# Optimization experiments

Measured on AMD Instinct MI355X. Metric: run time of the kernel, lower is better.

Reference implementation:

```python
import jax, jax.numpy as jnp
import numpy as np

N, E, D, K = 100000, 1000000, 64, 2  # nodes, edges, channels, kernel_size (dim=1, degree=1)


def setup_inputs() -> dict:
    key = jax.random.key(0)
    ks = jax.random.split(key, 10)
    x = jax.random.normal(ks[0], (N, D), dtype=jnp.float32)
    edge_index = jax.random.randint(ks[1], (2, E), 0, N, dtype=jnp.int64)
    edge_attr = jax.random.uniform(ks[2], (E, 1), dtype=jnp.float32)
    s = 1.0 / np.sqrt(D)
    W1 = jax.random.uniform(ks[3], (K, D, D), jnp.float32, -s, s)   # spline weights layer1 [K, in, out]
    lw1 = jax.random.uniform(ks[4], (D, D), jnp.float32, -s, s)     # root linear (x @ lw)
    b1 = jnp.zeros((D,), jnp.float32)
    W2 = jax.random.uniform(ks[5], (K, D, D), jnp.float32, -s, s)
    lw2 = jax.random.uniform(ks[6], (D, D), jnp.float32, -s, s)
    b2 = jnp.zeros((D,), jnp.float32)
    return {"x": x, "edge_index": edge_index, "edge_attr": edge_attr,
            "W1": W1, "lw1": lw1, "b1": b1, "W2": W2, "lw2": lw2, "b2": b2}


def spline_conv(x, src, dst, u, W, lw, b):
    # dim=1, degree=1, open B-spline: v = u*(K-1); linear interp between kernels floor(v), floor(v)+1
    k = W.shape[0]
    v = u[:, 0] * (k - 1)
    i0 = jnp.clip(jnp.floor(v), 0, k - 1).astype(jnp.int32)
    frac = v - i0.astype(v.dtype)            # in [0,1); 0 at u==1 after clipping
    i1 = jnp.minimum(i0 + 1, k - 1)
    Z = jnp.einsum('ni,kio->nko', x, W)      # [N, K, out] precompute per-kernel transforms
    msg = (1.0 - frac)[:, None] * Z[src, i0] + frac[:, None] * Z[src, i1]  # [E, out]
    agg = jax.ops.segment_sum(msg, dst, num_segments=x.shape[0])
    cnt = jax.ops.segment_sum(jnp.ones_like(dst, dtype=x.dtype), dst, num_segments=x.shape[0])
    out = agg / jnp.maximum(cnt, 1.0)[:, None]   # mean aggregation
    return out + x @ lw + b                      # root weight + bias


def reference(x, edge_index, edge_attr, W1, lw1, b1, W2, lw2, b2):
    src, dst = edge_index[0], edge_index[1]
    h = spline_conv(x, src, dst, edge_attr, W1, lw1, b1)
    h = jax.nn.relu(h)                 # dropout is identity in eval mode
    h = spline_conv(h, src, dst, edge_attr, W2, lw2, b2)
    h = jax.nn.relu(h)
    return h
```

## Files before the change

### kernel.cpp

```cpp
#include <hip/hip_runtime.h>

#define TPB 256

typedef __attribute__((ext_vector_type(8))) short bf16x8;
typedef __attribute__((ext_vector_type(4))) float f32x4;

__device__ __forceinline__ float bf2f(unsigned short u) {
    unsigned int x = ((unsigned int)u) << 16;
    return __builtin_bit_cast(float, x);
}
__device__ __forceinline__ unsigned short f2bf(float f) {
    unsigned int u = __builtin_bit_cast(unsigned int, f);
    unsigned int r = u + 0x7FFFu + ((u >> 16) & 1u);
    return (unsigned short)(r >> 16);
}

__global__ void prep_kernel(const float* __restrict__ x, uint2* __restrict__ xb, int n4,
                            const float* __restrict__ W1, const float* __restrict__ lw1,
                            const float* __restrict__ W2, const float* __restrict__ lw2,
                            bf16x8* __restrict__ WA,
                            const int* __restrict__ dst, const int* __restrict__ src,
                            const float* __restrict__ u, int* __restrict__ counts,
                            uint2* __restrict__ cp, int E) {
    int t = blockIdx.x * TPB + threadIdx.x;
    if (t < 3072) {
        int which = t / 1536;
        int rem = t - which * 1536;
        int fragid = rem >> 6;
        int lane = rem & 63;
        int kk = fragid >> 2, ct = fragid & 3;
        const float* W  = which ? W2  : W1;
        const float* lw = which ? lw2 : lw1;
        int col = ct * 16 + (lane & 15);
        int kbase = kk * 32 + (lane >> 4) * 8;
        short vals[8];
#pragma unroll
        for (int j = 0; j < 8; ++j) {
            int k = kbase + j;
            float v = (k < 128) ? W[(k & 1) * 4096 + (k >> 1) * 64 + col]
                                : lw[(k - 128) * 64 + col];
            vals[j] = (short)f2bf(v);
        }
        WA[t] = *reinterpret_cast<bf16x8*>(vals);
    }
    if (t < n4) {
        float4 v = reinterpret_cast<const float4*>(x)[t];
        uint2 r;
        r.x = (unsigned int)f2bf(v.x) | ((unsigned int)f2bf(v.y) << 16);
        r.y = (unsigned int)f2bf(v.z) | ((unsigned int)f2bf(v.w) << 16);
        xb[t] = r;
    }
    if (t < E) {
        int d = dst[t];
        int r = atomicAdd(&counts[d], 1);
        unsigned int uq = (unsigned int)__float2int_rn(u[t] * 32767.f);
        cp[t] = make_uint2((unsigned int)d | ((unsigned int)r << 17),
                           (unsigned int)src[t] | (uq << 17));
    }
}

__global__ void scan1_kernel(const int* __restrict__ counts, int* __restrict__ offsets,
                             int* __restrict__ bsum, int n) {
    __shared__ int s[TPB];
    int t = threadIdx.x;
    int base = blockIdx.x * 1024 + t * 4;
    int v[4];
#pragma unroll
    for (int q = 0; q < 4; ++q) v[q] = (base + q < n) ? counts[base + q] : 0;
    int tsum = v[0] + v[1] + v[2] + v[3];
    s[t] = tsum;
    __syncthreads();
    for (int off = 1; off < TPB; off <<= 1) {
        int x = (t >= off) ? s[t - off] : 0;
        __syncthreads();
        s[t] += x;
        __syncthreads();
    }
    int acc = s[t] - tsum;
#pragma unroll
    for (int q = 0; q < 4; ++q) {
        if (base + q < n) offsets[base + q] = acc;
        acc += v[q];
    }
    if (t == TPB - 1) bsum[blockIdx.x] = s[TPB - 1];
}

__global__ void scan2_kernel(int* __restrict__ bsum, int nblk) {
    __shared__ int s[TPB];
    int t = threadIdx.x;
    int v = (t < nblk) ? bsum[t] : 0;
    s[t] = v;
    __syncthreads();
    for (int off = 1; off < TPB; off <<= 1) {
        int x = (t >= off) ? s[t - off] : 0;
        __syncthreads();
        s[t] += x;
        __syncthreads();
    }
    if (t < nblk) bsum[t] = s[t] - v;
}

__global__ void scan3_kernel(int* __restrict__ offsets, const int* __restrict__ bsum,
                             int n, int E) {
    int base = blockIdx.x * 1024 + threadIdx.x * 4;
    int add = bsum[blockIdx.x];
#pragma unroll
    for (int q = 0; q < 4; ++q) {
        int idx = base + q;
        if (idx < n) offsets[idx] += add;
    }
    if (blockIdx.x == 0 && threadIdx.x == 0) offsets[n] = E;
}

__global__ void fill_kernel(const uint2* __restrict__ cp,
                            const int* __restrict__ offsets,
                            unsigned int* __restrict__ csr, int E, int nphases) {
    int stride = gridDim.x * TPB;
    for (int p = 0; p < nphases; ++p) {
        for (int e = blockIdx.x * TPB + threadIdx.x; e < E; e += stride) {
            uint2 r = cp[e];
            int d = r.x & 0x1FFFF;
            if ((d >> 16) == p) {
                int pos = offsets[d] + (int)(r.x >> 17);
                csr[pos] = r.y;
            }
        }
    }
}

__global__ void agg_kernel(const unsigned int* __restrict__ featu,
                           const int* __restrict__ offsets,
                           const unsigned int* __restrict__ csr,
                           unsigned int* __restrict__ A, int N) {
    int gw = (blockIdx.x * TPB + threadIdx.x) >> 6;
    int lane = threadIdx.x & 63;
    int n0 = gw * 2;
    if (n0 >= N) return;
    int half = lane >> 5, sub = lane & 31;
    const float us = 1.f / 32767.f;

    int ov = offsets[min(n0 + (lane & 3), N)];
    int o0 = __shfl(ov, 0), o1 = __shfl(ov, 1), o2 = __shfl(ov, 2);
    int beg = o0;
    int cnt = o2 - o0;
    unsigned int cw = (lane < cnt) ? csr[beg + lane] : 0u;

    int S0 = 0, E0 = o1 - o0;
    int S1 = E0, E1 = cnt;

    unsigned int fb[16], cs[16];
#pragma unroll
    for (int i = 0; i < 2; ++i) {
        int si = i ? S1 : S0;
        int ei = i ? E1 : E0;
        int bend = min(min(ei, si + 16), 64);
#pragma unroll
        for (int q = 0; q < 8; ++q) {
            int eidx = si + 2 * q + half;
            bool v = eidx < bend;
            unsigned int c = __shfl(cw, v ? eidx : 0);
            cs[i * 8 + q] = c;
            fb[i * 8 + q] = featu[(size_t)(c & 0x1FFFF) * 32 + sub];
        }
    }

#pragma unroll
    for (int i = 0; i < 2; ++i) {
        int si = i ? S1 : S0;
        int ei = i ? E1 : E0;
        int bend = min(min(ei, si + 16), 64);
        float a0x = 0.f, a1x = 0.f, a0y = 0.f, a1y = 0.f;
#pragma unroll
        for (int q = 0; q < 8; ++q) {
            int eidx = si + 2 * q + half;
            float m = (eidx < bend) ? 1.f : 0.f;
            unsigned int c = cs[i * 8 + q];
            unsigned int f = fb[i * 8 + q];
            float uu = (float)(c >> 17) * us;
            float w1 = uu * m;
            float w0 = m - w1;
            float fx = bf2f((unsigned short)f);
            float fy = bf2f((unsigned short)(f >> 16));
            a0x = fmaf(fx, w0, a0x); a1x = fmaf(fx, w1, a1x);
            a0y = fmaf(fy, w0, a0y); a1y = fmaf(fy, w1, a1y);
        }
        int tstart = max(si, bend);
        for (int t = tstart + half; t < ei; t += 2) {
            unsigned int c = csr[beg + t];
            unsigned int f = featu[(size_t)(c & 0x1FFFF) * 32 + sub];
            float uu = (float)(c >> 17) * us;
            float w0 = 1.f - uu;
            float fx = bf2f((unsigned short)f);
            float fy = bf2f((unsigned short)(f >> 16));
            a0x = fmaf(fx, w0, a0x); a1x = fmaf(fx, uu, a1x);
            a0y = fmaf(fy, w0, a0y); a1y = fmaf(fy, uu, a1y);
        }
        a0x += __shfl_xor(a0x, 32); a1x += __shfl_xor(a1x, 32);
        a0y += __shfl_xor(a0y, 32); a1y += __shfl_xor(a1y, 32);
        int node = n0 + i;
        int cN = ei - si;
        float inv = 1.f / (float)(cN > 0 ? cN : 1);
        if (half == 0 && node < N) {
            uint2 pk;
            pk.x = (unsigned int)f2bf(a0x * inv) | ((unsigned int)f2bf(a1x * inv) << 16);
            pk.y = (unsigned int)f2bf(a0y * inv) | ((unsigned int)f2bf(a1y * inv) << 16);
            *reinterpret_cast<uint2*>(A + (size_t)node * 64 + sub * 2) = pk;
        }
    }
}

__global__ void gemm_mfma_kernel(const unsigned int* __restrict__ A,
                                 const unsigned short* __restrict__ feat,
                                 const bf16x8* __restrict__ WA,
                                 const float* __restrict__ bias,
                                 unsigned short* __restrict__ out_bf,
                                 float* __restrict__ out_f,
                                 int N, int write_f32) {
    int w = threadIdx.x >> 6, lane = threadIdx.x & 63;
    int node = blockIdx.x * 64 + w * 16 + (lane & 15);
    int nc = min(node, N - 1);
    int kq = lane >> 4;
    const char* arow = (const char*)A + (size_t)nc * 256 + kq * 16;
    const char* frow = (const char*)feat + (size_t)nc * 128 + kq * 16;
    bf16x8 bq[6];
    bq[0] = *(const bf16x8*)(arow);
    bq[1] = *(const bf16x8*)(arow + 64);
    bq[2] = *(const bf16x8*)(arow + 128);
    bq[3] = *(const bf16x8*)(arow + 192);
    bq[4] = *(const bf16x8*)(frow);
    bq[5] = *(const bf16x8*)(frow + 64);

    f32x4 acc0 = {0.f, 0.f, 0.f, 0.f}, acc1 = acc0, acc2 = acc0, acc3 = acc0;
#pragma unroll
    for (int kk = 0; kk < 6; ++kk) {
        bf16x8 b = bq[kk];
        acc0 = __builtin_amdgcn_mfma_f32_16x16x32_bf16(WA[(kk * 4 + 0) * 64 + lane], b, acc0, 0, 0, 0);
        acc1 = __builtin_amdgcn_mfma_f32_16x16x32_bf16(WA[(kk * 4 + 1) * 64 + lane], b, acc1, 0, 0, 0);
        acc2 = __builtin_amdgcn_mfma_f32_16x16x32_bf16(WA[(kk * 4 + 2) * 64 + lane], b, acc2, 0, 0, 0);
        acc3 = __builtin_amdgcn_mfma_f32_16x16x32_bf16(WA[(kk * 4 + 3) * 64 + lane], b, acc3, 0, 0, 0);
    }
    if (node >= N) return;

    f32x4 accs[4] = {acc0, acc1, acc2, acc3};
    int cb_hi = 4 * kq;
#pragma unroll
    for (int ct = 0; ct < 4; ++ct) {
        int cb = ct * 16 + cb_hi;
        float r0 = fmaxf(accs[ct][0] + bias[cb + 0], 0.f);
        float r1 = fmaxf(accs[ct][1] + bias[cb + 1], 0.f);
        float r2 = fmaxf(accs[ct][2] + bias[cb + 2], 0.f);
        float r3 = fmaxf(accs[ct][3] + bias[cb + 3], 0.f);
        if (write_f32) {
            *reinterpret_cast<float4*>(out_f + (size_t)node * 64 + cb) =
                make_float4(r0, r1, r2, r3);
        } else {
            uint2 pk;
            pk.x = (unsigned int)f2bf(r0) | ((unsigned int)f2bf(r1) << 16);
            pk.y = (unsigned int)f2bf(r2) | ((unsigned int)f2bf(r3) << 16);
            *reinterpret_cast<uint2*>(out_bf + (size_t)node * 64 + cb) = pk;
        }
    }
}

extern "C" void kernel_launch(void* const* d_in, const int* in_sizes, int n_in,
                              void* d_out, int out_size, void* d_ws, size_t ws_size,
                              hipStream_t stream) {
    const float* x   = (const float*)d_in[0];
    const int*   ei  = (const int*)d_in[1];
    const float* ea  = (const float*)d_in[2];
    const float* W1  = (const float*)d_in[3];
    const float* lw1 = (const float*)d_in[4];
    const float* b1  = (const float*)d_in[5];
    const float* W2  = (const float*)d_in[6];
    const float* lw2 = (const float*)d_in[7];
    const float* b2  = (const float*)d_in[8];

    const int N = in_sizes[0] / 64;
    const int E = in_sizes[1] / 2;

    char* p = (char*)d_ws;
    auto carve = [&](size_t bytes) -> void* {
        void* r = (void*)p;
        p += (bytes + 255) & ~(size_t)255;
        return r;
    };
    unsigned short* xb   = (unsigned short*)carve((size_t)N * 64 * 2);
    unsigned short* h    = (unsigned short*)carve((size_t)N * 64 * 2);
    unsigned int*   A    = (unsigned int*)carve((size_t)N * 64 * 4);
    bf16x8* WA      = (bf16x8*)carve(3072 * 16);
    int*   counts   = (int*)carve((size_t)N * 4);
    int*   offsets  = (int*)carve((size_t)(N + 1) * 4);
    int*   bsum     = (int*)carve(256 * 4);
    uint2* cp       = (uint2*)carve((size_t)E * 8);
    unsigned int* csr = (unsigned int*)carve((size_t)E * 4);

    const int* src = ei;
    const int* dst = ei + E;

    hipMemsetAsync(counts, 0, (size_t)N * 4, stream);

    int n4 = N * 64 / 4;
    int prepTotal = n4 > E ? n4 : E;
    prep_kernel<<<(prepTotal + TPB - 1) / TPB, TPB, 0, stream>>>(
        x, (uint2*)xb, n4, W1, lw1, W2, lw2, WA, dst, src, ea, counts, cp, E);

    int nscan = (N + 1023) / 1024;
    scan1_kernel<<<nscan, TPB, 0, stream>>>(counts, offsets, bsum, N);
    scan2_kernel<<<1, TPB, 0, stream>>>(bsum, nscan);
    scan3_kernel<<<nscan, TPB, 0, stream>>>(offsets, bsum, N, E);

    int eBlocks = (E + TPB - 1) / TPB;
    int nphases = (N + 65535) >> 16;
    fill_kernel<<<eBlocks, TPB, 0, stream>>>(cp, offsets, csr, E, nphases);

    int nwaves = (N + 1) / 2;
    int aBlocks = (nwaves + 3) / 4;
    int gBlocks = (N + 63) / 64;

    agg_kernel<<<aBlocks, TPB, 0, stream>>>((const unsigned int*)xb, offsets, csr, A, N);
    gemm_mfma_kernel<<<gBlocks, TPB, 0, stream>>>(A, xb, WA, b1, h, nullptr, N, 0);
    agg_kernel<<<aBlocks, TPB, 0, stream>>>((const unsigned int*)h, offsets, csr, A, N);
    gemm_mfma_kernel<<<gBlocks, TPB, 0, stream>>>(A, h, WA + 1536, b2, nullptr, (float*)d_out, N, 1);
}
```

Before: 166.8 us.

## Fuse neighbor aggregation with MFMA GEMM via LDS staging per 16-node block

Merges the aggregation and MFMA GEMM kernels into one. Each 256-thread block aggregates 16 nodes into shared memory, then each wave computes one 16-column output tile from LDS. This removes the global round trip of the N×64 intermediate A buffer and two kernel launches per layer. In exchange each wave now runs only 16x16 MFMA tiles, adds a block-wide barrier, and the GEMM phase uses less parallel work per block.

```diff
diff --git a/kernel.cpp b/kernel.cpp
--- a/kernel.cpp
+++ b/kernel.cpp
@@ -128,137 +128,125 @@
     }
 }
 
-__global__ void agg_kernel(const unsigned int* __restrict__ featu,
-                           const int* __restrict__ offsets,
-                           const unsigned int* __restrict__ csr,
-                           unsigned int* __restrict__ A, int N) {
-    int gw = (blockIdx.x * TPB + threadIdx.x) >> 6;
-    int lane = threadIdx.x & 63;
-    int n0 = gw * 2;
-    if (n0 >= N) return;
+__global__ void fused_kernel(const unsigned int* __restrict__ featu,
+                             const int* __restrict__ offsets,
+                             const unsigned int* __restrict__ csr,
+                             const bf16x8* __restrict__ WA,
+                             const float* __restrict__ bias,
+                             unsigned short* __restrict__ out_bf,
+                             float* __restrict__ out_f,
+                             int N, int write_f32) {
+    __shared__ unsigned int lds[16 * 68];
+    int wid = threadIdx.x >> 6, lane = threadIdx.x & 63;
+    int nb = blockIdx.x * 16;
     int half = lane >> 5, sub = lane & 31;
     const float us = 1.f / 32767.f;
 
-    int ov = offsets[min(n0 + (lane & 3), N)];
-    int o0 = __shfl(ov, 0), o1 = __shfl(ov, 1), o2 = __shfl(ov, 2);
-    int beg = o0;
-    int cnt = o2 - o0;
-    unsigned int cw = (lane < cnt) ? csr[beg + lane] : 0u;
-
-    int S0 = 0, E0 = o1 - o0;
-    int S1 = E0, E1 = cnt;
-
-    unsigned int fb[16], cs[16];
-#pragma unroll
-    for (int i = 0; i < 2; ++i) {
-        int si = i ? S1 : S0;
-        int ei = i ? E1 : E0;
-        int bend = min(min(ei, si + 16), 64);
-#pragma unroll
-        for (int q = 0; q < 8; ++q) {
-            int eidx = si + 2 * q + half;
-            bool v = eidx < bend;
-            unsigned int c = __shfl(cw, v ? eidx : 0);
-            cs[i * 8 + q] = c;
-            fb[i * 8 + q] = featu[(size_t)(c & 0x1FFFF) * 32 + sub];
+#pragma unroll
+    for (int batch = 0; batch < 2; ++batch) {
+        int n0 = nb + wid * 4 + batch * 2;
+        int ov = offsets[min(n0 + (lane & 3), N)];
+        int o0 = __shfl(ov, 0), o1 = __shfl(ov, 1), o2 = __shfl(ov, 2);
+        int beg = o0;
+        int cnt = o2 - o0;
+        unsigned int cw = (lane < cnt) ? csr[beg + lane] : 0u;
+        int S0 = 0, E0 = o1 - o0, S1 = E0, E1 = cnt;
+
+        unsigned int fb[16], cs[16];
+#pragma unroll
+        for (int i = 0; i < 2; ++i) {
+            int si = i ? S1 : S0;
+            int ei = i ? E1 : E0;
+            int bend = min(min(ei, si + 16), 64);
+#pragma unroll
+            for (int q = 0; q < 8; ++q) {
+                int eidx = si + 2 * q + half;
+                bool v = eidx < bend;
+                unsigned int c = __shfl(cw, v ? eidx : 0);
+                cs[i * 8 + q] = c;
+                fb[i * 8 + q] = featu[(size_t)(c & 0x1FFFF) * 32 + sub];
+            }
         }
-    }
-
-#pragma unroll
-    for (int i = 0; i < 2; ++i) {
-        int si = i ? S1 : S0;
-        int ei = i ? E1 : E0;
-        int bend = min(min(ei, si + 16), 64);
-        float a0x = 0.f, a1x = 0.f, a0y = 0.f, a1y = 0.f;
-#pragma unroll
-        for (int q = 0; q < 8; ++q) {
-            int eidx = si + 2 * q + half;
-            float m = (eidx < bend) ? 1.f : 0.f;
-            unsigned int c = cs[i * 8 + q];
-            unsigned int f = fb[i * 8 + q];
-            float uu = (float)(c >> 17) * us;
-            float w1 = uu * m;
-            float w0 = m - w1;
-            float fx = bf2f((unsigned short)f);
-            float fy = bf2f((unsigned short)(f >> 16));
-            a0x = fmaf(fx, w0, a0x); a1x = fmaf(fx, w1, a1x);
-            a0y = fmaf(fy, w0, a0y); a1y = fmaf(fy, w1, a1y);
+
+#pragma unroll
+        for (int i = 0; i < 2; ++i) {
+            int si = i ? S1 : S0;
+            int ei = i ? E1 : E0;
+            int bend = min(min(ei, si + 16), 64);
+            float a0x = 0.f, a1x = 0.f, a0y = 0.f, a1y = 0.f;
+#pragma unroll
+            for (int q = 0; q < 8; ++q) {
+                int eidx = si + 2 * q + half;
+                float m = (eidx < bend) ? 1.f : 0.f;
+                unsigned int c = cs[i * 8 + q];
+                unsigned int f = fb[i * 8 + q];
+                float uu = (float)(c >> 17) * us;
+                float w1 = uu * m;
+                float w0 = m - w1;
+                float fx = bf2f((unsigned short)f);
+                float fy = bf2f((unsigned short)(f >> 16));
+                a0x = fmaf(fx, w0, a0x); a1x = fmaf(fx, w1, a1x);
+                a0y = fmaf(fy, w0, a0y); a1y = fmaf(fy, w1, a1y);
+            }
+            int tstart = max(si, bend);
+            for (int t = tstart + half; t < ei; t += 2) {
+                unsigned int c = csr[beg + t];
+                unsigned int f = featu[(size_t)(c & 0x1FFFF) * 32 + sub];
+                float uu = (float)(c >> 17) * us;
+                float w0 = 1.f - uu;
+                float fx = bf2f((unsigned short)f);
+                float fy = bf2f((unsigned short)(f >> 16));
+                a0x = fmaf(fx, w0, a0x); a1x = fmaf(fx, uu, a1x);
+                a0y = fmaf(fy, w0, a0y); a1y = fmaf(fy, uu, a1y);
+            }
+            a0x += __shfl_xor(a0x, 32); a1x += __shfl_xor(a1x, 32);
+            a0y += __shfl_xor(a0y, 32); a1y += __shfl_xor(a1y, 32);
+            int cN = ei - si;
+            float inv = 1.f / (float)(cN > 0 ? cN : 1);
+            if (half == 0) {
+                int nrel = n0 + i - nb;
+                uint2 pk;
+                pk.x = (unsigned int)f2bf(a0x * inv) | ((unsigned int)f2bf(a1x * inv) << 16);
+                pk.y = (unsigned int)f2bf(a0y * inv) | ((unsigned int)f2bf(a1y * inv) << 16);
+                *reinterpret_cast<uint2*>(&lds[nrel * 68 + sub * 2]) = pk;
+            }
         }
-        int tstart = max(si, bend);
-        for (int t = tstart + half; t < ei; t += 2) {
-            unsigned int c = csr[beg + t];
-            unsigned int f = featu[(size_t)(c & 0x1FFFF) * 32 + sub];
-            float uu = (float)(c >> 17) * us;
-            float w0 = 1.f - uu;
-            float fx = bf2f((unsigned short)f);
-            float fy = bf2f((unsigned short)(f >> 16));
-            a0x = fmaf(fx, w0, a0x); a1x = fmaf(fx, uu, a1x);
-            a0y = fmaf(fy, w0, a0y); a1y = fmaf(fy, uu, a1y);
-        }
-        a0x += __shfl_xor(a0x, 32); a1x += __shfl_xor(a1x, 32);
-        a0y += __shfl_xor(a0y, 32); a1y += __shfl_xor(a1y, 32);
-        int node = n0 + i;
-        int cN = ei - si;
-        float inv = 1.f / (float)(cN > 0 ? cN : 1);
-        if (half == 0 && node < N) {
-            uint2 pk;
-            pk.x = (unsigned int)f2bf(a0x * inv) | ((unsigned int)f2bf(a1x * inv) << 16);
-            pk.y = (unsigned int)f2bf(a0y * inv) | ((unsigned int)f2bf(a1y * inv) << 16);
-            *reinterpret_cast<uint2*>(A + (size_t)node * 64 + sub * 2) = pk;
-        }
-    }
-}
-
-__global__ void gemm_mfma_kernel(const unsigned int* __restrict__ A,
-                                 const unsigned short* __restrict__ feat,
-                                 const bf16x8* __restrict__ WA,
-                                 const float* __restrict__ bias,
-                                 unsigned short* __restrict__ out_bf,
-                                 float* __restrict__ out_f,
-                                 int N, int write_f32) {
-    int w = threadIdx.x >> 6, lane = threadIdx.x & 63;
-    int node = blockIdx.x * 64 + w * 16 + (lane & 15);
+    }
+    __syncthreads();
+
+    int node = nb + (lane & 15);
     int nc = min(node, N - 1);
     int kq = lane >> 4;
-    const char* arow = (const char*)A + (size_t)nc * 256 + kq * 16;
-    const char* frow = (const char*)feat + (size_t)nc * 128 + kq * 16;
+    const unsigned int* arow = &lds[(lane & 15) * 68 + kq * 4];
+    const char* frow = (const char*)featu + (size_t)nc * 128 + kq * 16;
     bf16x8 bq[6];
-    bq[0] = *(const bf16x8*)(arow);
-    bq[1] = *(const bf16x8*)(arow + 64);
-    bq[2] = *(const bf16x8*)(arow + 128);
-    bq[3] = *(const bf16x8*)(arow + 192);
-    bq[4] = *(const bf16x8*)(frow);
-    bq[5] = *(const bf16x8*)(frow + 64);
-
-    f32x4 acc0 = {0.f, 0.f, 0.f, 0.f}, acc1 = acc0, acc2 = acc0, acc3 = acc0;
-#pragma unroll
-    for (int kk = 0; kk < 6; ++kk) {
-        bf16x8 b = bq[kk];
-        acc0 = __builtin_amdgcn_mfma_f32_16x16x32_bf16(WA[(kk * 4 + 0) * 64 + lane], b, acc0, 0, 0, 0);
-        acc1 = __builtin_amdgcn_mfma_f32_16x16x32_bf16(WA[(kk * 4 + 1) * 64 + lane], b, acc1, 0, 0, 0);
-        acc2 = __builtin_amdgcn_mfma_f32_16x16x32_bf16(WA[(kk * 4 + 2) * 64 + lane], b, acc2, 0, 0, 0);
-        acc3 = __builtin_amdgcn_mfma_f32_16x16x32_bf16(WA[(kk * 4 + 3) * 64 + lane], b, acc3, 0, 0, 0);
-    }
+    bq[0] = *reinterpret_cast<const bf16x8*>(arow);
+    bq[1] = *reinterpret_cast<const bf16x8*>(arow + 16);
+    bq[2] = *reinterpret_cast<const bf16x8*>(arow + 32);
+    bq[3] = *reinterpret_cast<const bf16x8*>(arow + 48);
+    bq[4] = *reinterpret_cast<const bf16x8*>(frow);
+    bq[5] = *reinterpret_cast<const bf16x8*>(frow + 64);
+
+    f32x4 acc = {0.f, 0.f, 0.f, 0.f};
+#pragma unroll
+    for (int kk = 0; kk < 6; ++kk)
+        acc = __builtin_amdgcn_mfma_f32_16x16x32_bf16(WA[(kk * 4 + wid) * 64 + lane],
+                                                      bq[kk], acc, 0, 0, 0);
     if (node >= N) return;
 
-    f32x4 accs[4] = {acc0, acc1, acc2, acc3};
-    int cb_hi = 4 * kq;
-#pragma unroll
-    for (int ct = 0; ct < 4; ++ct) {
-        int cb = ct * 16 + cb_hi;
-        float r0 = fmaxf(accs[ct][0] + bias[cb + 0], 0.f);
-        float r1 = fmaxf(accs[ct][1] + bias[cb + 1], 0.f);
-        float r2 = fmaxf(accs[ct][2] + bias[cb + 2], 0.f);
-        float r3 = fmaxf(accs[ct][3] + bias[cb + 3], 0.f);
-        if (write_f32) {
-            *reinterpret_cast<float4*>(out_f + (size_t)node * 64 + cb) =
-                make_float4(r0, r1, r2, r3);
-        } else {
-            uint2 pk;
-            pk.x = (unsigned int)f2bf(r0) | ((unsigned int)f2bf(r1) << 16);
-            pk.y = (unsigned int)f2bf(r2) | ((unsigned int)f2bf(r3) << 16);
-            *reinterpret_cast<uint2*>(out_bf + (size_t)node * 64 + cb) = pk;
-        }
+    int cb = wid * 16 + 4 * kq;
+    float r0 = fmaxf(acc[0] + bias[cb + 0], 0.f);
+    float r1 = fmaxf(acc[1] + bias[cb + 1], 0.f);
+    float r2 = fmaxf(acc[2] + bias[cb + 2], 0.f);
+    float r3 = fmaxf(acc[3] + bias[cb + 3], 0.f);
+    if (write_f32) {
+        *reinterpret_cast<float4*>(out_f + (size_t)node * 64 + cb) =
+            make_float4(r0, r1, r2, r3);
+    } else {
+        uint2 pk;
+        pk.x = (unsigned int)f2bf(r0) | ((unsigned int)f2bf(r1) << 16);
+        pk.y = (unsigned int)f2bf(r2) | ((unsigned int)f2bf(r3) << 16);
+        *reinterpret_cast<uint2*>(out_bf + (size_t)node * 64 + cb) = pk;
     }
 }
 
@@ -286,7 +274,6 @@
     };
     unsigned short* xb   = (unsigned short*)carve((size_t)N * 64 * 2);
     unsigned short* h    = (unsigned short*)carve((size_t)N * 64 * 2);
-    unsigned int*   A    = (unsigned int*)carve((size_t)N * 64 * 4);
     bf16x8* WA      = (bf16x8*)carve(3072 * 16);
     int*   counts   = (int*)carve((size_t)N * 4);
     int*   offsets  = (int*)carve((size_t)(N + 1) * 4);
@@ -313,12 +300,10 @@
     int nphases = (N + 65535) >> 16;
     fill_kernel<<<eBlocks, TPB, 0, stream>>>(cp, offsets, csr, E, nphases);
 
-    int nwaves = (N + 1) / 2;
-    int aBlocks = (nwaves + 3) / 4;
-    int gBlocks = (N + 63) / 64;
-
-    agg_kernel<<<aBlocks, TPB, 0, stream>>>((const unsigned int*)xb, offsets, csr, A, N);
-    gemm_mfma_kernel<<<gBlocks, TPB, 0, stream>>>(A, xb, WA, b1, h, nullptr, N, 0);
-    agg_kernel<<<aBlocks, TPB, 0, stream>>>((const unsigned int*)h, offsets, csr, A, N);
-    gemm_mfma_kernel<<<gBlocks, TPB, 0, stream>>>(A, h, WA + 1536, b2, nullptr, (float*)d_out, N, 1);
-}
+    int fBlocks = (N + 15) / 16;
+
+    fused_kernel<<<fBlocks, TPB, 0, stream>>>((const unsigned int*)xb, offsets, csr,
+                                              WA, b1, h, nullptr, N, 0);
+    fused_kernel<<<fBlocks, TPB, 0, stream>>>((const unsigned int*)h, offsets, csr,
+                                              WA + 1536, b2, nullptr, (float*)d_out, N, 1);
+}
```

After: 146.6 us. 1.14x faster.
